# Kernel optimization log

Measured on AMD Instinct MI355X. Metric: run time of the kernel, lower is better.

Reference implementation:

```python
import jax, jax.numpy as jnp
import numpy as np

B, C, H, W = 4, 512, 32, 32
NUM_HEADS, DIM_HEAD = 16, 32
DIM_ATTN = NUM_HEADS * DIM_HEAD  # 512
N = H * W


def setup_inputs() -> dict:
    key = jax.random.key(0)
    ks = jax.random.split(key, 6)
    s = 0.02
    return {
        "x": jax.random.normal(ks[0], (B, C, H, W), jnp.float32),
        "w_qkv": jax.random.normal(ks[1], (3 * DIM_ATTN, C), jnp.float32) * s,
        "b_qkv": jax.random.normal(ks[2], (3 * DIM_ATTN,), jnp.float32) * s,
        "w_proj": jax.random.normal(ks[3], (C, DIM_ATTN), jnp.float32) * s,
        "b_proj": jax.random.normal(ks[4], (C,), jnp.float32) * s,
        "shared_rel_pos": jax.random.normal(ks[5], (1, NUM_HEADS, N, N), jnp.float32) * s,
    }


def reference(x, w_qkv, b_qkv, w_proj, b_proj, shared_rel_pos):
    b, c, h, w = x.shape
    n = h * w
    scale = DIM_HEAD ** -0.5
    # 1x1 conv == per-pixel matmul over channels
    qkv = jnp.einsum('bchw,oc->bohw', x, w_qkv) + b_qkv[None, :, None, None]
    # [B, heads, 3*dh, N] -> chunk along dim 2 (matches torch .chunk(3, dim=2))
    qkv = qkv.reshape(b, NUM_HEADS, 3 * DIM_HEAD, n)
    q, k, v = jnp.split(qkv, 3, axis=2)          # each [B, heads, dh, N]
    attn = jnp.einsum('bhdi,bhdj->bhij', q, k) * scale  # q^T @ k
    attn = attn + shared_rel_pos
    attn = jax.nn.softmax(attn, axis=-1)
    out = jnp.einsum('bhdj,bhij->bhdi', v, attn)  # v @ attn^T, [B, heads, dh, N]
    out = out.reshape(b, NUM_HEADS * DIM_HEAD, h, w)
    out = jnp.einsum('bchw,oc->bohw', out, w_proj) + b_proj[None, :, None, None]
    return out
```

## Files before the change

### kernel.cpp

```cpp
#include <hip/hip_runtime.h>
#include <cstdint>
#include <cstddef>

#define BATCH 4
#define CIN   512
#define NPIX  1024
#define HEADS 16
#define DH    32
#define DATTN 512
#define O_QKV 1536

typedef unsigned short u16;
typedef __bf16 bf16x4 __attribute__((ext_vector_type(4)));
typedef __bf16 bf16x8 __attribute__((ext_vector_type(8)));
typedef float  f32x4  __attribute__((ext_vector_type(4)));

typedef const __attribute__((address_space(1))) void g1_t;
typedef __attribute__((address_space(3))) void l3_t;

#if defined(__has_builtin)
#if __has_builtin(__builtin_amdgcn_exp2f)
#define EXP2(x) __builtin_amdgcn_exp2f(x)
#endif
#endif
#ifndef EXP2
#define EXP2(x) __expf((x) * 0.6931471805599453f)
#endif

__device__ __forceinline__ u16 f2bf(float f) {
  unsigned u = __float_as_uint(f);
  u += 0x7fffu + ((u >> 16) & 1u);
  return (u16)(u >> 16);
}

__device__ __forceinline__ void gl_lds16(const void* gp, void* lp) {
  __builtin_amdgcn_global_load_lds((g1_t*)gp, (l3_t*)lp, 16, 0, 0);
}

__global__ __launch_bounds__(256) void prep_w(const float* __restrict__ w1,
                                              const float* __restrict__ w2,
                                              u16* __restrict__ o1,
                                              u16* __restrict__ o2) {
  const int idx = blockIdx.x * 256 + threadIdx.x;
  const int n1 = (O_QKV * CIN) >> 2;
  float4 v = (idx < n1) ? reinterpret_cast<const float4*>(w1)[idx]
                        : reinterpret_cast<const float4*>(w2)[idx - n1];
  uint2 pk = make_uint2((unsigned)f2bf(v.x) | ((unsigned)f2bf(v.y) << 16),
                        (unsigned)f2bf(v.z) | ((unsigned)f2bf(v.w) << 16));
  if (idx < n1) reinterpret_cast<uint2*>(o1)[idx] = pk;
  else          reinterpret_cast<uint2*>(o2)[idx - n1] = pk;
}

__global__ __launch_bounds__(256) void prep_x(const float* __restrict__ x,
                                              u16* __restrict__ xt) {
  __shared__ float sT[64][65];
  const int t  = threadIdx.x;
  const int n0 = blockIdx.x * 64;
  const int c0 = blockIdx.y * 64;
  const int b  = blockIdx.z;
  const float* xb = x + ((size_t)b * CIN + c0) * NPIX + n0;
#pragma unroll
  for (int i = 0; i < 4; ++i) {
    int r   = i * 16 + (t >> 4);
    int col = (t & 15) << 2;
    float4 v = *reinterpret_cast<const float4*>(&xb[(size_t)r * NPIX + col]);
    sT[r][col + 0] = v.x; sT[r][col + 1] = v.y;
    sT[r][col + 2] = v.z; sT[r][col + 3] = v.w;
  }
  __syncthreads();
#pragma unroll
  for (int i = 0; i < 2; ++i) {
    int nl = t >> 2;
    int ch = (t & 3) + (i << 2);
    u16 tmp[8];
#pragma unroll
    for (int e = 0; e < 8; ++e) tmp[e] = f2bf(sT[(ch << 3) + e][nl]);
    *reinterpret_cast<uint4*>(&xt[((size_t)b * NPIX + n0 + nl) * CIN + c0 + (ch << 3)]) =
        *reinterpret_cast<uint4*>(tmp);
  }
}

__global__ __launch_bounds__(256) void gemm_qkv_mfma(const u16* __restrict__ wq,
                                                     const u16* __restrict__ xt,
                                                     const float* __restrict__ bias,
                                                     u16* __restrict__ qt,
                                                     u16* __restrict__ kt,
                                                     u16* __restrict__ vt) {
  __shared__ __align__(16) u16 sA[96 * 64];
  __shared__ __align__(16) u16 sB[128 * 64];
  const int t  = threadIdx.x;
  const int w  = t >> 6, l = t & 63, g = l >> 4, ln = l & 15;
  const int n0 = blockIdx.x * 128;
  const int h  = blockIdx.y;
  const int b  = blockIdx.z;
  const int wm = w >> 1, wn = w & 1;

  const u16* wbase = wq + (size_t)h * 96 * CIN;
  const u16* xbase = xt + ((size_t)b * NPIX + n0) * CIN;

  f32x4 acc[3][4];
#pragma unroll
  for (int mi = 0; mi < 3; ++mi)
#pragma unroll
    for (int ni = 0; ni < 4; ++ni) acc[mi][ni] = {0.f, 0.f, 0.f, 0.f};

  for (int k0 = 0; k0 < CIN; k0 += 64) {
#pragma unroll
    for (int i = 0; i < 3; ++i) {
      int chunk = i * 256 + (w << 6) + l;
      gl_lds16(wbase + ((size_t)(chunk >> 3)) * CIN + k0 + ((chunk & 7) << 3),
               (char*)sA + i * 4096 + (w << 10));
    }
#pragma unroll
    for (int i = 0; i < 4; ++i) {
      int chunk = i * 256 + (w << 6) + l;
      gl_lds16(xbase + ((size_t)(chunk >> 3)) * CIN + k0 + ((chunk & 7) << 3),
               (char*)sB + i * 4096 + (w << 10));
    }
    __syncthreads();
#pragma unroll
    for (int kk = 0; kk < 64; kk += 32) {
      bf16x8 af[3], bfr[4];
#pragma unroll
      for (int mi = 0; mi < 3; ++mi)
        af[mi] = *reinterpret_cast<const bf16x8*>(&sA[(48 * wm + 16 * mi + ln) * 64 + kk + (g << 3)]);
#pragma unroll
      for (int ni = 0; ni < 4; ++ni)
        bfr[ni] = *reinterpret_cast<const bf16x8*>(&sB[((wn << 6) + (ni << 4) + ln) * 64 + kk + (g << 3)]);
#pragma unroll
      for (int mi = 0; mi < 3; ++mi)
#pragma unroll
        for (int ni = 0; ni < 4; ++ni)
          acc[mi][ni] = __builtin_amdgcn_mfma_f32_16x16x32_bf16(af[mi], bfr[ni], acc[mi][ni], 0, 0, 0);
    }
    __syncthreads();
  }

  const float QSC = 0.17677669529663687f * 1.4426950408889634f;
  const float* bh = bias + h * 96;
#pragma unroll
  for (int mi = 0; mi < 3; ++mi) {
    const int sec = 48 * wm + 16 * mi;
    const int rb  = sec + (g << 2);
    const float b0 = bh[rb + 0], b1 = bh[rb + 1], b2 = bh[rb + 2], b3 = bh[rb + 3];
#pragma unroll
    for (int ni = 0; ni < 4; ++ni) {
      const int n = n0 + (wn << 6) + (ni << 4) + ln;
      f32x4 a = acc[mi][ni];
      float v0 = a[0] + b0, v1 = a[1] + b1, v2 = a[2] + b2, v3 = a[3] + b3;
      if (sec < 32) { v0 *= QSC; v1 *= QSC; v2 *= QSC; v3 *= QSC; }
      u16 e0 = f2bf(v0), e1 = f2bf(v1), e2 = f2bf(v2), e3 = f2bf(v3);
      if (sec < 32) {
        const int d = sec + (g << 2);
        uint2 pk = make_uint2((unsigned)e0 | ((unsigned)e1 << 16),
                              (unsigned)e2 | ((unsigned)e3 << 16));
        *reinterpret_cast<uint2*>(&qt[(((size_t)(b * HEADS + h)) * NPIX + n) * DH + d]) = pk;
      } else if (sec < 64) {
        const int d = sec - 32 + (g << 2);
        uint2 pk = make_uint2((unsigned)e0 | ((unsigned)e1 << 16),
                              (unsigned)e2 | ((unsigned)e3 << 16));
        *reinterpret_cast<uint2*>(&kt[(((size_t)(b * HEADS + h)) * NPIX + n) * DH + d]) = pk;
      } else {
        const int d = sec - 64 + (g << 2);
        u16* vp = &vt[(((size_t)(b * HEADS + h)) * DH + d) * NPIX + n];
        vp[0] = e0; vp[NPIX] = e1; vp[2 * NPIX] = e2; vp[3 * NPIX] = e3;
      }
    }
  }
}

__global__ __launch_bounds__(256, 4) void attn_mfma(const u16* __restrict__ qt,
                                                    const u16* __restrict__ kt,
                                                    const u16* __restrict__ vt,
                                                    const float* __restrict__ rel,
                                                    u16* __restrict__ aout) {
  __shared__ __align__(16) u16 sK[2][2048];
  __shared__ __align__(16) u16 sV[2][2048];
  __shared__ __align__(16) u16 sP[4][1024];

  const int t  = threadIdx.x;
  const int w  = t >> 6, l = t & 63, g = l >> 4, ln = l & 15;
  const int bid = blockIdx.x;
  const int xcd = bid & 7, sl = bid >> 3;
  const int b   = sl & 3;
  const int i0  = ((sl >> 2) & 15) << 6;
  const int h   = (xcd << 1) | (sl >> 6);
  const int iw  = w;

  const size_t bh = (size_t)(b * HEADS + h);

  const int sc_r  = t >> 3;
  const int sc_kc = (t & 7) ^ (sc_r & 7) ^ ((sc_r >> 3) & 1);
  const int sc_vc = (t & 7) ^ (sc_r & 7);
  const u16* ksrc = kt + (bh * NPIX + ((sc_r << 1) | (sc_kc >> 2))) * DH +
                    ((sc_kc & 3) << 3);
  const u16* vsrc = vt + (bh * DH + sc_r) * NPIX + (sc_vc << 3);
  char* kdst = (char*)&sK[0][0] + (w << 10);
  char* vdst = (char*)&sV[0][0] + (w << 10);

#define STAGE(s_, p_) do {                                          \
    gl_lds16(ksrc + (size_t)(s_) * 2048, kdst + (p_) * 4096);       \
    gl_lds16(vsrc + (size_t)(s_) * 64,   vdst + (p_) * 4096);       \
  } while (0)

  STAGE(0, 0);

  bf16x8 qf = *reinterpret_cast<const bf16x8*>(
      qt + (bh * NPIX + i0 + (iw << 4) + ln) * DH + (g << 3));

  const float* relp = rel + ((size_t)h * NPIX + i0 + (iw << 4) + (g << 2)) * NPIX +
                      (ln << 2);
  f32x4 relA4[4], relB4[4];
#pragma unroll
  for (int v = 0; v < 4; ++v)
    relA4[v] = *reinterpret_cast<const f32x4*>(relp + (size_t)v * NPIX);

  f32x4 vzero = {0.f, 0.f, 0.f, 0.f};
  f32x4 accO[2] = {vzero, vzero};
  f32x4 l_lane = vzero;

  u16* sPw = &sP[w][0];
  const float LOG2E = 1.4426950408889634f;

  for (int s = 0; s < 16; ++s) {
    const int p = s & 1;
    __syncthreads();
    if (s < 15) {
      STAGE(s + 1, p ^ 1);
#pragma unroll
      for (int v = 0; v < 4; ++v)
        relB4[v] = *reinterpret_cast<const f32x4*>(relp + (size_t)v * NPIX + ((s + 1) << 6));
    }

    const u16* Kb = &sK[p][0];
    const u16* Vb = &sV[p][0];

    f32x4 sfr[4];
    __builtin_amdgcn_s_setprio(1);
#pragma unroll
    for (int jj = 0; jj < 4; ++jj) {
      const int r  = (ln << 1) + (jj >> 1);
      const int ks = ((((jj & 1) << 2) | g) ^ (r & 7)) ^ ((r >> 3) & 1);
      bf16x8 kf = *reinterpret_cast<const bf16x8*>(Kb + r * 64 + ks * 8);
      sfr[jj] = __builtin_amdgcn_mfma_f32_16x16x32_bf16(qf, kf, vzero, 0, 0, 0);
    }
    __builtin_amdgcn_s_setprio(0);

#pragma unroll
    for (int v = 0; v < 4; ++v) {
      float p0 = EXP2(fmaf(relA4[v][0], LOG2E, sfr[0][v]));
      float p1 = EXP2(fmaf(relA4[v][1], LOG2E, sfr[1][v]));
      float p2 = EXP2(fmaf(relA4[v][2], LOG2E, sfr[2][v]));
      float p3 = EXP2(fmaf(relA4[v][3], LOG2E, sfr[3][v]));
      l_lane[v] += (p0 + p1) + (p2 + p3);
      bf16x4 pk;
      pk[0] = (__bf16)p0; pk[1] = (__bf16)p1; pk[2] = (__bf16)p2; pk[3] = (__bf16)p3;
      const int rw = (g << 2) + v;
      *reinterpret_cast<bf16x4*>(
          sPw + rw * 64 + ((((ln >> 1) ^ (rw & 7)) << 3) | ((ln & 1) << 2))) = pk;
    }

    __builtin_amdgcn_s_setprio(1);
#pragma unroll
    for (int kc = 0; kc < 2; ++kc) {
      const int lc = (kc << 2) | g;
      bf16x8 pa = *reinterpret_cast<const bf16x8*>(sPw + ln * 64 + ((lc ^ (ln & 7)) << 3));
#pragma unroll
      for (int dc = 0; dc < 2; ++dc) {
        const int d  = (dc << 4) + ln;
        const int vs = lc ^ (d & 7);
        bf16x8 vf = *reinterpret_cast<const bf16x8*>(Vb + d * 64 + vs * 8);
        accO[dc] = __builtin_amdgcn_mfma_f32_16x16x32_bf16(pa, vf, accO[dc], 0, 0, 0);
      }
    }
    __builtin_amdgcn_s_setprio(0);

    if (s < 15) {
#pragma unroll
      for (int v = 0; v < 4; ++v) relA4[v] = relB4[v];
    }
  }
#undef STAGE

#pragma unroll
  for (int v = 0; v < 4; ++v) {
    float ls = l_lane[v];
    ls += __shfl_xor(ls, 1);
    ls += __shfl_xor(ls, 2);
    ls += __shfl_xor(ls, 4);
    ls += __shfl_xor(ls, 8);
    const float inv = 1.f / ls;
    const size_t row = (size_t)b * NPIX + i0 + (iw << 4) + (g << 2) + v;
    aout[row * DATTN + (h << 5) + ln]      = f2bf(accO[0][v] * inv);
    aout[row * DATTN + (h << 5) + 16 + ln] = f2bf(accO[1][v] * inv);
  }
}

__global__ __launch_bounds__(256) void gemm_proj_mfma(const u16* __restrict__ wp,
                                                      const u16* __restrict__ at,
                                                      const float* __restrict__ bias,
                                                      float* __restrict__ out) {
  __shared__ __align__(16) u16 sA[64 * 64];
  __shared__ __align__(16) u16 sB[128 * 64];
  const int t  = threadIdx.x;
  const int w  = t >> 6, l = t & 63, g = l >> 4, ln = l & 15;
  const int n0 = blockIdx.x * 128;
  const int o0 = blockIdx.y * 64;
  const int b  = blockIdx.z;
  const int wm = w >> 1, wn = w & 1;

  const u16* wbase = wp + (size_t)o0 * DATTN;
  const u16* abase = at + ((size_t)b * NPIX + n0) * DATTN;

  f32x4 acc[2][4];
#pragma unroll
  for (int mi = 0; mi < 2; ++mi)
#pragma unroll
    for (int ni = 0; ni < 4; ++ni) acc[mi][ni] = {0.f, 0.f, 0.f, 0.f};

  for (int k0 = 0; k0 < DATTN; k0 += 64) {
#pragma unroll
    for (int i = 0; i < 2; ++i) {
      int chunk = i * 256 + (w << 6) + l;
      gl_lds16(wbase + ((size_t)(chunk >> 3)) * DATTN + k0 + ((chunk & 7) << 3),
               (char*)sA + i * 4096 + (w << 10));
    }
#pragma unroll
    for (int i = 0; i < 4; ++i) {
      int chunk = i * 256 + (w << 6) + l;
      gl_lds16(abase + ((size_t)(chunk >> 3)) * DATTN + k0 + ((chunk & 7) << 3),
               (char*)sB + i * 4096 + (w << 10));
    }
    __syncthreads();
#pragma unroll
    for (int kk = 0; kk < 64; kk += 32) {
      bf16x8 af[2], bfr[4];
#pragma unroll
      for (int mi = 0; mi < 2; ++mi)
        af[mi] = *reinterpret_cast<const bf16x8*>(&sA[((wm << 5) + (mi << 4) + ln) * 64 + kk + (g << 3)]);
#pragma unroll
      for (int ni = 0; ni < 4; ++ni)
        bfr[ni] = *reinterpret_cast<const bf16x8*>(&sB[((wn << 6) + (ni << 4) + ln) * 64 + kk + (g << 3)]);
#pragma unroll
      for (int mi = 0; mi < 2; ++mi)
#pragma unroll
        for (int ni = 0; ni < 4; ++ni)
          acc[mi][ni] = __builtin_amdgcn_mfma_f32_16x16x32_bf16(af[mi], bfr[ni], acc[mi][ni], 0, 0, 0);
    }
    __syncthreads();
  }

#pragma unroll
  for (int mi = 0; mi < 2; ++mi) {
    const int o = o0 + (wm << 5) + (mi << 4) + (g << 2);
    const float b0 = bias[o], b1 = bias[o + 1], b2 = bias[o + 2], b3 = bias[o + 3];
#pragma unroll
    for (int ni = 0; ni < 4; ++ni) {
      const int n = n0 + (wn << 6) + (ni << 4) + ln;
      float* op = &out[((size_t)b * DATTN + o) * NPIX + n];
      op[0]        = acc[mi][ni][0] + b0;
      op[NPIX]     = acc[mi][ni][1] + b1;
      op[2 * NPIX] = acc[mi][ni][2] + b2;
      op[3 * NPIX] = acc[mi][ni][3] + b3;
    }
  }
}

extern "C" void kernel_launch(void* const* d_in, const int* in_sizes, int n_in,
                              void* d_out, int out_size, void* d_ws, size_t ws_size,
                              hipStream_t stream) {
  (void)in_sizes; (void)n_in; (void)out_size; (void)ws_size;
  const float* x      = (const float*)d_in[0];
  const float* w_qkv  = (const float*)d_in[1];
  const float* b_qkv  = (const float*)d_in[2];
  const float* w_proj = (const float*)d_in[3];
  const float* b_proj = (const float*)d_in[4];
  const float* rel    = (const float*)d_in[5];
  float* out = (float*)d_out;

  u16* xt    = (u16*)d_ws;
  u16* wq_bf = xt + (size_t)BATCH * NPIX * CIN;
  u16* wp_bf = wq_bf + (size_t)O_QKV * CIN;
  u16* qt    = wp_bf + (size_t)DATTN * DATTN;
  u16* kt    = qt + (size_t)BATCH * HEADS * NPIX * DH;
  u16* vt    = kt + (size_t)BATCH * HEADS * NPIX * DH;
  u16* aout  = vt + (size_t)BATCH * HEADS * NPIX * DH;

  prep_w<<<1024, 256, 0, stream>>>(w_qkv, w_proj, wq_bf, wp_bf);
  prep_x<<<dim3(NPIX / 64, CIN / 64, BATCH), 256, 0, stream>>>(x, xt);
  gemm_qkv_mfma<<<dim3(NPIX / 128, HEADS, BATCH), 256, 0, stream>>>(wq_bf, xt, b_qkv, qt, kt, vt);
  attn_mfma<<<1024, 256, 0, stream>>>(qt, kt, vt, rel, aout);
  gemm_proj_mfma<<<dim3(NPIX / 128, DATTN / 64, BATCH), 256, 0, stream>>>(wp_bf, aout, b_proj, out);
}
```

Measured before the change: 63.92 us.

## Load K and V fragments directly from global into registers, dropping LDS staging

The attention kernel no longer stages K and V tiles through double-buffered shared memory with async global-to-LDS copies and a per-step __syncthreads. Each wave now reads its MFMA K fragments (prefetched one step ahead into registers) and V fragments straight from global memory. This removes LDS traffic and block-wide barriers, but each of the four waves now fetches the same K/V data separately, and V loads are issued in the same iteration they are used, so there is less reuse and more latency exposure on L2/global reads. Register pressure also rises with the extra prefetch fragments.

Result: slower. 104.4 us (+63.2%).

```diff
diff --git a/kernel.cpp b/kernel.cpp
--- a/kernel.cpp
+++ b/kernel.cpp
@@ -174,8 +174,6 @@
                                                     const u16* __restrict__ vt,
                                                     const float* __restrict__ rel,
                                                     u16* __restrict__ aout) {
-  __shared__ __align__(16) u16 sK[2][2048];
-  __shared__ __align__(16) u16 sV[2][2048];
   __shared__ __align__(16) u16 sP[4][1024];
 
   const int t  = threadIdx.x;
@@ -189,31 +187,14 @@
 
   const size_t bh = (size_t)(b * HEADS + h);
 
-  const int sc_r  = t >> 3;
-  const int sc_kc = (t & 7) ^ (sc_r & 7) ^ ((sc_r >> 3) & 1);
-  const int sc_vc = (t & 7) ^ (sc_r & 7);
-  const u16* ksrc = kt + (bh * NPIX + ((sc_r << 1) | (sc_kc >> 2))) * DH +
-                    ((sc_kc & 3) << 3);
-  const u16* vsrc = vt + (bh * DH + sc_r) * NPIX + (sc_vc << 3);
-  char* kdst = (char*)&sK[0][0] + (w << 10);
-  char* vdst = (char*)&sV[0][0] + (w << 10);
-
-#define STAGE(s_, p_) do {                                          \
-    gl_lds16(ksrc + (size_t)(s_) * 2048, kdst + (p_) * 4096);       \
-    gl_lds16(vsrc + (size_t)(s_) * 64,   vdst + (p_) * 4096);       \
-  } while (0)
-
-  STAGE(0, 0);
-
   bf16x8 qf = *reinterpret_cast<const bf16x8*>(
       qt + (bh * NPIX + i0 + (iw << 4) + ln) * DH + (g << 3));
 
+  const u16* kbase = kt + (bh * NPIX + (ln << 2)) * DH + (g << 3);
+  const u16* vbase0 = vt + (bh * DH + ln) * NPIX + (g << 3);
+  const u16* vbase1 = vbase0 + 16 * NPIX;
   const float* relp = rel + ((size_t)h * NPIX + i0 + (iw << 4) + (g << 2)) * NPIX +
                       (ln << 2);
-  f32x4 relA4[4], relB4[4];
-#pragma unroll
-  for (int v = 0; v < 4; ++v)
-    relA4[v] = *reinterpret_cast<const f32x4*>(relp + (size_t)v * NPIX);
 
   f32x4 vzero = {0.f, 0.f, 0.f, 0.f};
   f32x4 accO[2] = {vzero, vzero};
@@ -222,36 +203,51 @@
   u16* sPw = &sP[w][0];
   const float LOG2E = 1.4426950408889634f;
 
+  const int paOff0 = ln * 64 + ((g ^ (ln & 7)) << 3);
+  const int paOff1 = ln * 64 + (((4 | g) ^ (ln & 7)) << 3);
+
+  bf16x8 kA0, kA1, kA2, kA3, kB0, kB1, kB2, kB3;
+  f32x4 relA4[4], relB4[4];
+  kA0 = *reinterpret_cast<const bf16x8*>(kbase);
+  kA1 = *reinterpret_cast<const bf16x8*>(kbase + DH);
+  kA2 = *reinterpret_cast<const bf16x8*>(kbase + 2 * DH);
+  kA3 = *reinterpret_cast<const bf16x8*>(kbase + 3 * DH);
+#pragma unroll
+  for (int v = 0; v < 4; ++v)
+    relA4[v] = *reinterpret_cast<const f32x4*>(relp + (size_t)v * NPIX);
+
   for (int s = 0; s < 16; ++s) {
-    const int p = s & 1;
-    __syncthreads();
     if (s < 15) {
-      STAGE(s + 1, p ^ 1);
+      const u16* kn = kbase + (size_t)(s + 1) * 64 * DH;
+      kB0 = *reinterpret_cast<const bf16x8*>(kn);
+      kB1 = *reinterpret_cast<const bf16x8*>(kn + DH);
+      kB2 = *reinterpret_cast<const bf16x8*>(kn + 2 * DH);
+      kB3 = *reinterpret_cast<const bf16x8*>(kn + 3 * DH);
 #pragma unroll
       for (int v = 0; v < 4; ++v)
         relB4[v] = *reinterpret_cast<const f32x4*>(relp + (size_t)v * NPIX + ((s + 1) << 6));
     }
-
-    const u16* Kb = &sK[p][0];
-    const u16* Vb = &sV[p][0];
-
-    f32x4 sfr[4];
+    const u16* vp0 = vbase0 + (s << 6);
+    const u16* vp1 = vbase1 + (s << 6);
+    bf16x8 vf00 = *reinterpret_cast<const bf16x8*>(vp0);
+    bf16x8 vf01 = *reinterpret_cast<const bf16x8*>(vp1);
+    bf16x8 vf10 = *reinterpret_cast<const bf16x8*>(vp0 + 32);
+    bf16x8 vf11 = *reinterpret_cast<const bf16x8*>(vp1 + 32);
+
+    f32x4 sfr0, sfr1, sfr2, sfr3;
     __builtin_amdgcn_s_setprio(1);
-#pragma unroll
-    for (int jj = 0; jj < 4; ++jj) {
-      const int r  = (ln << 1) + (jj >> 1);
-      const int ks = ((((jj & 1) << 2) | g) ^ (r & 7)) ^ ((r >> 3) & 1);
-      bf16x8 kf = *reinterpret_cast<const bf16x8*>(Kb + r * 64 + ks * 8);
-      sfr[jj] = __builtin_amdgcn_mfma_f32_16x16x32_bf16(qf, kf, vzero, 0, 0, 0);
-    }
+    sfr0 = __builtin_amdgcn_mfma_f32_16x16x32_bf16(qf, kA0, vzero, 0, 0, 0);
+    sfr1 = __builtin_amdgcn_mfma_f32_16x16x32_bf16(qf, kA1, vzero, 0, 0, 0);
+    sfr2 = __builtin_amdgcn_mfma_f32_16x16x32_bf16(qf, kA2, vzero, 0, 0, 0);
+    sfr3 = __builtin_amdgcn_mfma_f32_16x16x32_bf16(qf, kA3, vzero, 0, 0, 0);
     __builtin_amdgcn_s_setprio(0);
 
 #pragma unroll
     for (int v = 0; v < 4; ++v) {
-      float p0 = EXP2(fmaf(relA4[v][0], LOG2E, sfr[0][v]));
-      float p1 = EXP2(fmaf(relA4[v][1], LOG2E, sfr[1][v]));
-      float p2 = EXP2(fmaf(relA4[v][2], LOG2E, sfr[2][v]));
-      float p3 = EXP2(fmaf(relA4[v][3], LOG2E, sfr[3][v]));
+      float p0 = EXP2(fmaf(relA4[v][0], LOG2E, sfr0[v]));
+      float p1 = EXP2(fmaf(relA4[v][1], LOG2E, sfr1[v]));
+      float p2 = EXP2(fmaf(relA4[v][2], LOG2E, sfr2[v]));
+      float p3 = EXP2(fmaf(relA4[v][3], LOG2E, sfr3[v]));
       l_lane[v] += (p0 + p1) + (p2 + p3);
       bf16x4 pk;
       pk[0] = (__bf16)p0; pk[1] = (__bf16)p1; pk[2] = (__bf16)p2; pk[3] = (__bf16)p3;
@@ -261,26 +257,22 @@
     }
 
     __builtin_amdgcn_s_setprio(1);
-#pragma unroll
-    for (int kc = 0; kc < 2; ++kc) {
-      const int lc = (kc << 2) | g;
-      bf16x8 pa = *reinterpret_cast<const bf16x8*>(sPw + ln * 64 + ((lc ^ (ln & 7)) << 3));
-#pragma unroll
-      for (int dc = 0; dc < 2; ++dc) {
-        const int d  = (dc << 4) + ln;
-        const int vs = lc ^ (d & 7);
-        bf16x8 vf = *reinterpret_cast<const bf16x8*>(Vb + d * 64 + vs * 8);
-        accO[dc] = __builtin_amdgcn_mfma_f32_16x16x32_bf16(pa, vf, accO[dc], 0, 0, 0);
-      }
+    {
+      bf16x8 pa0 = *reinterpret_cast<const bf16x8*>(sPw + paOff0);
+      accO[0] = __builtin_amdgcn_mfma_f32_16x16x32_bf16(pa0, vf00, accO[0], 0, 0, 0);
+      accO[1] = __builtin_amdgcn_mfma_f32_16x16x32_bf16(pa0, vf01, accO[1], 0, 0, 0);
+      bf16x8 pa1 = *reinterpret_cast<const bf16x8*>(sPw + paOff1);
+      accO[0] = __builtin_amdgcn_mfma_f32_16x16x32_bf16(pa1, vf10, accO[0], 0, 0, 0);
+      accO[1] = __builtin_amdgcn_mfma_f32_16x16x32_bf16(pa1, vf11, accO[1], 0, 0, 0);
     }
     __builtin_amdgcn_s_setprio(0);
 
     if (s < 15) {
+      kA0 = kB0; kA1 = kB1; kA2 = kB2; kA3 = kB3;
 #pragma unroll
       for (int v = 0; v < 4; ++v) relA4[v] = relB4[v];
     }
   }
-#undef STAGE
 
 #pragma unroll
   for (int v = 0; v < 4; ++v) {
```

## Fuse prep kernels and double attention key tile per pipeline stage

Applied to the files above, without the earlier changes.

Merges the weight-cast and x-transpose prep kernels into one launch, removing a kernel launch and its gap. In the attention kernel, each pipeline stage now covers 128 keys instead of 64, halving the number of barrier-synchronized iterations and issuing more MFMAs per sync. The rel-pos bias is now loaded synchronously inside each iteration instead of being prefetched one stage ahead, which may expose global latency. LDS use doubles, which can reduce occupancy.

After: 63.93 us. About the same (+0.0%).

```diff
diff --git a/kernel.cpp b/kernel.cpp
--- a/kernel.cpp
+++ b/kernel.cpp
@@ -37,46 +37,48 @@
   __builtin_amdgcn_global_load_lds((g1_t*)gp, (l3_t*)lp, 16, 0, 0);
 }
 
-__global__ __launch_bounds__(256) void prep_w(const float* __restrict__ w1,
-                                              const float* __restrict__ w2,
-                                              u16* __restrict__ o1,
-                                              u16* __restrict__ o2) {
-  const int idx = blockIdx.x * 256 + threadIdx.x;
-  const int n1 = (O_QKV * CIN) >> 2;
-  float4 v = (idx < n1) ? reinterpret_cast<const float4*>(w1)[idx]
-                        : reinterpret_cast<const float4*>(w2)[idx - n1];
-  uint2 pk = make_uint2((unsigned)f2bf(v.x) | ((unsigned)f2bf(v.y) << 16),
-                        (unsigned)f2bf(v.z) | ((unsigned)f2bf(v.w) << 16));
-  if (idx < n1) reinterpret_cast<uint2*>(o1)[idx] = pk;
-  else          reinterpret_cast<uint2*>(o2)[idx - n1] = pk;
-}
-
-__global__ __launch_bounds__(256) void prep_x(const float* __restrict__ x,
-                                              u16* __restrict__ xt) {
-  __shared__ float sT[64][65];
-  const int t  = threadIdx.x;
-  const int n0 = blockIdx.x * 64;
-  const int c0 = blockIdx.y * 64;
-  const int b  = blockIdx.z;
-  const float* xb = x + ((size_t)b * CIN + c0) * NPIX + n0;
-#pragma unroll
-  for (int i = 0; i < 4; ++i) {
-    int r   = i * 16 + (t >> 4);
-    int col = (t & 15) << 2;
-    float4 v = *reinterpret_cast<const float4*>(&xb[(size_t)r * NPIX + col]);
-    sT[r][col + 0] = v.x; sT[r][col + 1] = v.y;
-    sT[r][col + 2] = v.z; sT[r][col + 3] = v.w;
-  }
-  __syncthreads();
-#pragma unroll
-  for (int i = 0; i < 2; ++i) {
-    int nl = t >> 2;
-    int ch = (t & 3) + (i << 2);
-    u16 tmp[8];
-#pragma unroll
-    for (int e = 0; e < 8; ++e) tmp[e] = f2bf(sT[(ch << 3) + e][nl]);
-    *reinterpret_cast<uint4*>(&xt[((size_t)b * NPIX + n0 + nl) * CIN + c0 + (ch << 3)]) =
-        *reinterpret_cast<uint4*>(tmp);
+__global__ __launch_bounds__(256) void prep_fused(const float* __restrict__ x,
+                                                  const float* __restrict__ w1,
+                                                  const float* __restrict__ w2,
+                                                  u16* __restrict__ xt,
+                                                  u16* __restrict__ o1,
+                                                  u16* __restrict__ o2) {
+  const int t = threadIdx.x;
+  if (blockIdx.x < 512) {
+    __shared__ float sT[64][65];
+    const int q  = blockIdx.x;
+    const int n0 = (q & 15) << 6;
+    const int c0 = ((q >> 4) & 7) << 6;
+    const int b  = q >> 7;
+    const float* xb = x + ((size_t)b * CIN + c0) * NPIX + n0;
+#pragma unroll
+    for (int i = 0; i < 4; ++i) {
+      int r   = i * 16 + (t >> 4);
+      int col = (t & 15) << 2;
+      float4 v = *reinterpret_cast<const float4*>(&xb[(size_t)r * NPIX + col]);
+      sT[r][col + 0] = v.x; sT[r][col + 1] = v.y;
+      sT[r][col + 2] = v.z; sT[r][col + 3] = v.w;
+    }
+    __syncthreads();
+#pragma unroll
+    for (int i = 0; i < 2; ++i) {
+      int nl = t >> 2;
+      int ch = (t & 3) + (i << 2);
+      u16 tmp[8];
+#pragma unroll
+      for (int e = 0; e < 8; ++e) tmp[e] = f2bf(sT[(ch << 3) + e][nl]);
+      *reinterpret_cast<uint4*>(&xt[((size_t)b * NPIX + n0 + nl) * CIN + c0 + (ch << 3)]) =
+          *reinterpret_cast<uint4*>(tmp);
+    }
+  } else {
+    const int idx = (blockIdx.x - 512) * 256 + t;
+    const int n1 = (O_QKV * CIN) >> 2;
+    float4 v = (idx < n1) ? reinterpret_cast<const float4*>(w1)[idx]
+                          : reinterpret_cast<const float4*>(w2)[idx - n1];
+    uint2 pk = make_uint2((unsigned)f2bf(v.x) | ((unsigned)f2bf(v.y) << 16),
+                          (unsigned)f2bf(v.z) | ((unsigned)f2bf(v.w) << 16));
+    if (idx < n1) reinterpret_cast<uint2*>(o1)[idx] = pk;
+    else          reinterpret_cast<uint2*>(o2)[idx - n1] = pk;
   }
 }
 
@@ -174,9 +176,9 @@
                                                     const u16* __restrict__ vt,
                                                     const float* __restrict__ rel,
                                                     u16* __restrict__ aout) {
-  __shared__ __align__(16) u16 sK[2][2048];
-  __shared__ __align__(16) u16 sV[2][2048];
-  __shared__ __align__(16) u16 sP[4][1024];
+  __shared__ __align__(16) u16 sK[2][4096];
+  __shared__ __align__(16) u16 sV[2][4096];
+  __shared__ __align__(16) u16 sP[4][2048];
 
   const int t  = threadIdx.x;
   const int w  = t >> 6, l = t & 63, g = l >> 4, ln = l & 15;
@@ -198,9 +200,11 @@
   char* kdst = (char*)&sK[0][0] + (w << 10);
   char* vdst = (char*)&sV[0][0] + (w << 10);
 
-#define STAGE(s_, p_) do {                                          \
-    gl_lds16(ksrc + (size_t)(s_) * 2048, kdst + (p_) * 4096);       \
-    gl_lds16(vsrc + (size_t)(s_) * 64,   vdst + (p_) * 4096);       \
+#define STAGE(s_, p_) do {                                                  \
+    gl_lds16(ksrc + (size_t)(s_) * 4096,        kdst + (p_) * 8192);        \
+    gl_lds16(ksrc + (size_t)(s_) * 4096 + 2048, kdst + (p_) * 8192 + 4096); \
+    gl_lds16(vsrc + (size_t)(s_) * 128,         vdst + (p_) * 8192);        \
+    gl_lds16(vsrc + (size_t)(s_) * 128 + 64,    vdst + (p_) * 8192 + 4096); \
   } while (0)
 
   STAGE(0, 0);
@@ -210,10 +214,6 @@
 
   const float* relp = rel + ((size_t)h * NPIX + i0 + (iw << 4) + (g << 2)) * NPIX +
                       (ln << 2);
-  f32x4 relA4[4], relB4[4];
-#pragma unroll
-  for (int v = 0; v < 4; ++v)
-    relA4[v] = *reinterpret_cast<const f32x4*>(relp + (size_t)v * NPIX);
 
   f32x4 vzero = {0.f, 0.f, 0.f, 0.f};
   f32x4 accO[2] = {vzero, vzero};
@@ -222,63 +222,72 @@
   u16* sPw = &sP[w][0];
   const float LOG2E = 1.4426950408889634f;
 
-  for (int s = 0; s < 16; ++s) {
+  for (int s = 0; s < 8; ++s) {
     const int p = s & 1;
     __syncthreads();
-    if (s < 15) {
-      STAGE(s + 1, p ^ 1);
+    if (s < 7) STAGE(s + 1, p ^ 1);
+
+    f32x4 relv[2][4];
+#pragma unroll
+    for (int hh = 0; hh < 2; ++hh)
 #pragma unroll
       for (int v = 0; v < 4; ++v)
-        relB4[v] = *reinterpret_cast<const f32x4*>(relp + (size_t)v * NPIX + ((s + 1) << 6));
-    }
+        relv[hh][v] = *reinterpret_cast<const f32x4*>(
+            relp + (size_t)v * NPIX + (s << 7) + (hh << 6));
 
     const u16* Kb = &sK[p][0];
     const u16* Vb = &sV[p][0];
 
-    f32x4 sfr[4];
+    f32x4 sfr[8];
     __builtin_amdgcn_s_setprio(1);
 #pragma unroll
-    for (int jj = 0; jj < 4; ++jj) {
-      const int r  = (ln << 1) + (jj >> 1);
-      const int ks = ((((jj & 1) << 2) | g) ^ (r & 7)) ^ ((r >> 3) & 1);
-      bf16x8 kf = *reinterpret_cast<const bf16x8*>(Kb + r * 64 + ks * 8);
+    for (int jj = 0; jj < 8; ++jj) {
+      const int hh = jj >> 2, q = jj & 3;
+      const int r  = (ln << 1) + (q >> 1);
+      const int ks = ((((q & 1) << 2) | g) ^ (r & 7)) ^ ((r >> 3) & 1);
+      bf16x8 kf = *reinterpret_cast<const bf16x8*>(Kb + (hh << 11) + r * 64 + ks * 8);
       sfr[jj] = __builtin_amdgcn_mfma_f32_16x16x32_bf16(qf, kf, vzero, 0, 0, 0);
     }
     __builtin_amdgcn_s_setprio(0);
 
 #pragma unroll
     for (int v = 0; v < 4; ++v) {
-      float p0 = EXP2(fmaf(relA4[v][0], LOG2E, sfr[0][v]));
-      float p1 = EXP2(fmaf(relA4[v][1], LOG2E, sfr[1][v]));
-      float p2 = EXP2(fmaf(relA4[v][2], LOG2E, sfr[2][v]));
-      float p3 = EXP2(fmaf(relA4[v][3], LOG2E, sfr[3][v]));
+      const int rw = (g << 2) + v;
+      const int pwoff = rw * 64 + ((((ln >> 1) ^ (rw & 7)) << 3) | ((ln & 1) << 2));
+      float p0 = EXP2(fmaf(relv[0][v][0], LOG2E, sfr[0][v]));
+      float p1 = EXP2(fmaf(relv[0][v][1], LOG2E, sfr[1][v]));
+      float p2 = EXP2(fmaf(relv[0][v][2], LOG2E, sfr[2][v]));
+      float p3 = EXP2(fmaf(relv[0][v][3], LOG2E, sfr[3][v]));
       l_lane[v] += (p0 + p1) + (p2 + p3);
       bf16x4 pk;
       pk[0] = (__bf16)p0; pk[1] = (__bf16)p1; pk[2] = (__bf16)p2; pk[3] = (__bf16)p3;
-      const int rw = (g << 2) + v;
-      *reinterpret_cast<bf16x4*>(
-          sPw + rw * 64 + ((((ln >> 1) ^ (rw & 7)) << 3) | ((ln & 1) << 2))) = pk;
+      *reinterpret_cast<bf16x4*>(sPw + pwoff) = pk;
+      float p4 = EXP2(fmaf(relv[1][v][0], LOG2E, sfr[4][v]));
+      float p5 = EXP2(fmaf(relv[1][v][1], LOG2E, sfr[5][v]));
+      float p6 = EXP2(fmaf(relv[1][v][2], LOG2E, sfr[6][v]));
+      float p7 = EXP2(fmaf(relv[1][v][3], LOG2E, sfr[7][v]));
+      l_lane[v] += (p4 + p5) + (p6 + p7);
+      bf16x4 pk2;
+      pk2[0] = (__bf16)p4; pk2[1] = (__bf16)p5; pk2[2] = (__bf16)p6; pk2[3] = (__bf16)p7;
+      *reinterpret_cast<bf16x4*>(sPw + 1024 + pwoff) = pk2;
     }
 
     __builtin_amdgcn_s_setprio(1);
 #pragma unroll
-    for (int kc = 0; kc < 2; ++kc) {
-      const int lc = (kc << 2) | g;
-      bf16x8 pa = *reinterpret_cast<const bf16x8*>(sPw + ln * 64 + ((lc ^ (ln & 7)) << 3));
+    for (int c = 0; c < 4; ++c) {
+      const int hh = c >> 1, kc2 = c & 1;
+      const int lc = (kc2 << 2) | g;
+      bf16x8 pa = *reinterpret_cast<const bf16x8*>(
+          sPw + (hh << 10) + ln * 64 + ((lc ^ (ln & 7)) << 3));
 #pragma unroll
       for (int dc = 0; dc < 2; ++dc) {
         const int d  = (dc << 4) + ln;
         const int vs = lc ^ (d & 7);
-        bf16x8 vf = *reinterpret_cast<const bf16x8*>(Vb + d * 64 + vs * 8);
+        bf16x8 vf = *reinterpret_cast<const bf16x8*>(Vb + (hh << 11) + d * 64 + vs * 8);
         accO[dc] = __builtin_amdgcn_mfma_f32_16x16x32_bf16(pa, vf, accO[dc], 0, 0, 0);
       }
     }
     __builtin_amdgcn_s_setprio(0);
-
-    if (s < 15) {
-#pragma unroll
-      for (int v = 0; v < 4; ++v) relA4[v] = relB4[v];
-    }
   }
 #undef STAGE
 
@@ -386,8 +395,7 @@
   u16* vt    = kt + (size_t)BATCH * HEADS * NPIX * DH;
   u16* aout  = vt + (size_t)BATCH * HEADS * NPIX * DH;
 
-  prep_w<<<1024, 256, 0, stream>>>(w_qkv, w_proj, wq_bf, wp_bf);
-  prep_x<<<dim3(NPIX / 64, CIN / 64, BATCH), 256, 0, stream>>>(x, xt);
+  prep_fused<<<1536, 256, 0, stream>>>(x, w_qkv, w_proj, xt, wq_bf, wp_bf);
   gemm_qkv_mfma<<<dim3(NPIX / 128, HEADS, BATCH), 256, 0, stream>>>(wq_bf, xt, b_qkv, qt, kt, vt);
   attn_mfma<<<1024, 256, 0, stream>>>(qt, kt, vt, rel, aout);
   gemm_proj_mfma<<<dim3(NPIX / 128, DATTN / 64, BATCH), 256, 0, stream>>>(wp_bf, aout, b_proj, out);
```

## Share rel_pos loads across two batches per attention block and fuse prep kernels

Applied to the files above, without the earlier changes.

Each attention block now handles two batch elements for the same head and query tile. The shared_rel_pos fp32 tile is therefore read once and reused for both, which halves traffic on the largest input. The grid shrinks to 512 blocks, LDS for K/V doubles, and launch bounds drop to 2 waves, so occupancy and parallelism go down. The weight and x bf16 preparation kernels are also merged into one launch to save a kernel launch.

New measurement: 62.74 us. Within noise of the previous version (-1.8%).

```diff
diff --git a/kernel.cpp b/kernel.cpp
--- a/kernel.cpp
+++ b/kernel.cpp
@@ -37,46 +37,48 @@
   __builtin_amdgcn_global_load_lds((g1_t*)gp, (l3_t*)lp, 16, 0, 0);
 }
 
-__global__ __launch_bounds__(256) void prep_w(const float* __restrict__ w1,
-                                              const float* __restrict__ w2,
-                                              u16* __restrict__ o1,
-                                              u16* __restrict__ o2) {
-  const int idx = blockIdx.x * 256 + threadIdx.x;
-  const int n1 = (O_QKV * CIN) >> 2;
-  float4 v = (idx < n1) ? reinterpret_cast<const float4*>(w1)[idx]
-                        : reinterpret_cast<const float4*>(w2)[idx - n1];
-  uint2 pk = make_uint2((unsigned)f2bf(v.x) | ((unsigned)f2bf(v.y) << 16),
-                        (unsigned)f2bf(v.z) | ((unsigned)f2bf(v.w) << 16));
-  if (idx < n1) reinterpret_cast<uint2*>(o1)[idx] = pk;
-  else          reinterpret_cast<uint2*>(o2)[idx - n1] = pk;
-}
-
-__global__ __launch_bounds__(256) void prep_x(const float* __restrict__ x,
-                                              u16* __restrict__ xt) {
-  __shared__ float sT[64][65];
-  const int t  = threadIdx.x;
-  const int n0 = blockIdx.x * 64;
-  const int c0 = blockIdx.y * 64;
-  const int b  = blockIdx.z;
-  const float* xb = x + ((size_t)b * CIN + c0) * NPIX + n0;
-#pragma unroll
-  for (int i = 0; i < 4; ++i) {
-    int r   = i * 16 + (t >> 4);
-    int col = (t & 15) << 2;
-    float4 v = *reinterpret_cast<const float4*>(&xb[(size_t)r * NPIX + col]);
-    sT[r][col + 0] = v.x; sT[r][col + 1] = v.y;
-    sT[r][col + 2] = v.z; sT[r][col + 3] = v.w;
-  }
-  __syncthreads();
-#pragma unroll
-  for (int i = 0; i < 2; ++i) {
-    int nl = t >> 2;
-    int ch = (t & 3) + (i << 2);
-    u16 tmp[8];
-#pragma unroll
-    for (int e = 0; e < 8; ++e) tmp[e] = f2bf(sT[(ch << 3) + e][nl]);
-    *reinterpret_cast<uint4*>(&xt[((size_t)b * NPIX + n0 + nl) * CIN + c0 + (ch << 3)]) =
-        *reinterpret_cast<uint4*>(tmp);
+__global__ __launch_bounds__(256) void prep_fused(const float* __restrict__ x,
+                                                  const float* __restrict__ w1,
+                                                  const float* __restrict__ w2,
+                                                  u16* __restrict__ xt,
+                                                  u16* __restrict__ o1,
+                                                  u16* __restrict__ o2) {
+  const int t = threadIdx.x;
+  if (blockIdx.x < 512) {
+    __shared__ float sT[64][65];
+    const int q  = blockIdx.x;
+    const int n0 = (q & 15) << 6;
+    const int c0 = ((q >> 4) & 7) << 6;
+    const int b  = q >> 7;
+    const float* xb = x + ((size_t)b * CIN + c0) * NPIX + n0;
+#pragma unroll
+    for (int i = 0; i < 4; ++i) {
+      int r   = i * 16 + (t >> 4);
+      int col = (t & 15) << 2;
+      float4 v = *reinterpret_cast<const float4*>(&xb[(size_t)r * NPIX + col]);
+      sT[r][col + 0] = v.x; sT[r][col + 1] = v.y;
+      sT[r][col + 2] = v.z; sT[r][col + 3] = v.w;
+    }
+    __syncthreads();
+#pragma unroll
+    for (int i = 0; i < 2; ++i) {
+      int nl = t >> 2;
+      int ch = (t & 3) + (i << 2);
+      u16 tmp[8];
+#pragma unroll
+      for (int e = 0; e < 8; ++e) tmp[e] = f2bf(sT[(ch << 3) + e][nl]);
+      *reinterpret_cast<uint4*>(&xt[((size_t)b * NPIX + n0 + nl) * CIN + c0 + (ch << 3)]) =
+          *reinterpret_cast<uint4*>(tmp);
+    }
+  } else {
+    const int idx = (blockIdx.x - 512) * 256 + t;
+    const int n1 = (O_QKV * CIN) >> 2;
+    float4 v = (idx < n1) ? reinterpret_cast<const float4*>(w1)[idx]
+                          : reinterpret_cast<const float4*>(w2)[idx - n1];
+    uint2 pk = make_uint2((unsigned)f2bf(v.x) | ((unsigned)f2bf(v.y) << 16),
+                          (unsigned)f2bf(v.z) | ((unsigned)f2bf(v.w) << 16));
+    if (idx < n1) reinterpret_cast<uint2*>(o1)[idx] = pk;
+    else          reinterpret_cast<uint2*>(o2)[idx - n1] = pk;
   }
 }
 
@@ -169,44 +171,51 @@
   }
 }
 
-__global__ __launch_bounds__(256, 4) void attn_mfma(const u16* __restrict__ qt,
+__global__ __launch_bounds__(256, 2) void attn_mfma(const u16* __restrict__ qt,
                                                     const u16* __restrict__ kt,
                                                     const u16* __restrict__ vt,
                                                     const float* __restrict__ rel,
                                                     u16* __restrict__ aout) {
-  __shared__ __align__(16) u16 sK[2][2048];
-  __shared__ __align__(16) u16 sV[2][2048];
+  __shared__ __align__(16) u16 sK[2][2][2048];
+  __shared__ __align__(16) u16 sV[2][2][2048];
   __shared__ __align__(16) u16 sP[4][1024];
 
   const int t  = threadIdx.x;
   const int w  = t >> 6, l = t & 63, g = l >> 4, ln = l & 15;
   const int bid = blockIdx.x;
   const int xcd = bid & 7, sl = bid >> 3;
-  const int b   = sl & 3;
-  const int i0  = ((sl >> 2) & 15) << 6;
-  const int h   = (xcd << 1) | (sl >> 6);
+  const int bp  = sl & 1;
+  const int i0  = ((sl >> 1) & 15) << 6;
+  const int h   = (xcd << 1) | (sl >> 5);
   const int iw  = w;
 
-  const size_t bh = (size_t)(b * HEADS + h);
+  const size_t bh0 = (size_t)((bp * 2 + 0) * HEADS + h);
+  const size_t bh1 = (size_t)((bp * 2 + 1) * HEADS + h);
 
   const int sc_r  = t >> 3;
   const int sc_kc = (t & 7) ^ (sc_r & 7) ^ ((sc_r >> 3) & 1);
   const int sc_vc = (t & 7) ^ (sc_r & 7);
-  const u16* ksrc = kt + (bh * NPIX + ((sc_r << 1) | (sc_kc >> 2))) * DH +
-                    ((sc_kc & 3) << 3);
-  const u16* vsrc = vt + (bh * DH + sc_r) * NPIX + (sc_vc << 3);
-  char* kdst = (char*)&sK[0][0] + (w << 10);
-  char* vdst = (char*)&sV[0][0] + (w << 10);
-
-#define STAGE(s_, p_) do {                                          \
-    gl_lds16(ksrc + (size_t)(s_) * 2048, kdst + (p_) * 4096);       \
-    gl_lds16(vsrc + (size_t)(s_) * 64,   vdst + (p_) * 4096);       \
+  const size_t kro = ((size_t)((sc_r << 1) | (sc_kc >> 2))) * DH + ((sc_kc & 3) << 3);
+  const u16* ksrc0 = kt + bh0 * NPIX * DH + kro;
+  const u16* ksrc1 = kt + bh1 * NPIX * DH + kro;
+  const u16* vsrc0 = vt + (bh0 * DH + sc_r) * NPIX + (sc_vc << 3);
+  const u16* vsrc1 = vt + (bh1 * DH + sc_r) * NPIX + (sc_vc << 3);
+  char* kBase = (char*)&sK[0][0][0] + (w << 10);
+  char* vBase = (char*)&sV[0][0][0] + (w << 10);
+
+#define STAGE(s_, p_) do {                                               \
+    gl_lds16(ksrc0 + (size_t)(s_) * 2048, kBase + (p_) * 8192);          \
+    gl_lds16(ksrc1 + (size_t)(s_) * 2048, kBase + (p_) * 8192 + 4096);   \
+    gl_lds16(vsrc0 + (size_t)(s_) * 64,   vBase + (p_) * 8192);          \
+    gl_lds16(vsrc1 + (size_t)(s_) * 64,   vBase + (p_) * 8192 + 4096);   \
   } while (0)
 
   STAGE(0, 0);
 
-  bf16x8 qf = *reinterpret_cast<const bf16x8*>(
-      qt + (bh * NPIX + i0 + (iw << 4) + ln) * DH + (g << 3));
+  bf16x8 qf0 = *reinterpret_cast<const bf16x8*>(
+      qt + (bh0 * NPIX + i0 + (iw << 4) + ln) * DH + (g << 3));
+  bf16x8 qf1 = *reinterpret_cast<const bf16x8*>(
+      qt + (bh1 * NPIX + i0 + (iw << 4) + ln) * DH + (g << 3));
 
   const float* relp = rel + ((size_t)h * NPIX + i0 + (iw << 4) + (g << 2)) * NPIX +
                       (ln << 2);
@@ -216,8 +225,9 @@
     relA4[v] = *reinterpret_cast<const f32x4*>(relp + (size_t)v * NPIX);
 
   f32x4 vzero = {0.f, 0.f, 0.f, 0.f};
-  f32x4 accO[2] = {vzero, vzero};
-  f32x4 l_lane = vzero;
+  f32x4 accO0[2] = {vzero, vzero};
+  f32x4 accO1[2] = {vzero, vzero};
+  f32x4 l_lane0 = vzero, l_lane1 = vzero;
 
   u16* sPw = &sP[w][0];
   const float LOG2E = 1.4426950408889634f;
@@ -232,48 +242,54 @@
         relB4[v] = *reinterpret_cast<const f32x4*>(relp + (size_t)v * NPIX + ((s + 1) << 6));
     }
 
-    const u16* Kb = &sK[p][0];
-    const u16* Vb = &sV[p][0];
-
-    f32x4 sfr[4];
-    __builtin_amdgcn_s_setprio(1);
-#pragma unroll
-    for (int jj = 0; jj < 4; ++jj) {
-      const int r  = (ln << 1) + (jj >> 1);
-      const int ks = ((((jj & 1) << 2) | g) ^ (r & 7)) ^ ((r >> 3) & 1);
-      bf16x8 kf = *reinterpret_cast<const bf16x8*>(Kb + r * 64 + ks * 8);
-      sfr[jj] = __builtin_amdgcn_mfma_f32_16x16x32_bf16(qf, kf, vzero, 0, 0, 0);
-    }
-    __builtin_amdgcn_s_setprio(0);
-
-#pragma unroll
-    for (int v = 0; v < 4; ++v) {
-      float p0 = EXP2(fmaf(relA4[v][0], LOG2E, sfr[0][v]));
-      float p1 = EXP2(fmaf(relA4[v][1], LOG2E, sfr[1][v]));
-      float p2 = EXP2(fmaf(relA4[v][2], LOG2E, sfr[2][v]));
-      float p3 = EXP2(fmaf(relA4[v][3], LOG2E, sfr[3][v]));
-      l_lane[v] += (p0 + p1) + (p2 + p3);
-      bf16x4 pk;
-      pk[0] = (__bf16)p0; pk[1] = (__bf16)p1; pk[2] = (__bf16)p2; pk[3] = (__bf16)p3;
-      const int rw = (g << 2) + v;
-      *reinterpret_cast<bf16x4*>(
-          sPw + rw * 64 + ((((ln >> 1) ^ (rw & 7)) << 3) | ((ln & 1) << 2))) = pk;
-    }
-
-    __builtin_amdgcn_s_setprio(1);
-#pragma unroll
-    for (int kc = 0; kc < 2; ++kc) {
-      const int lc = (kc << 2) | g;
-      bf16x8 pa = *reinterpret_cast<const bf16x8*>(sPw + ln * 64 + ((lc ^ (ln & 7)) << 3));
-#pragma unroll
-      for (int dc = 0; dc < 2; ++dc) {
-        const int d  = (dc << 4) + ln;
-        const int vs = lc ^ (d & 7);
-        bf16x8 vf = *reinterpret_cast<const bf16x8*>(Vb + d * 64 + vs * 8);
-        accO[dc] = __builtin_amdgcn_mfma_f32_16x16x32_bf16(pa, vf, accO[dc], 0, 0, 0);
+#pragma unroll
+    for (int b2 = 0; b2 < 2; ++b2) {
+      const u16* Kb = &sK[p][b2][0];
+      const u16* Vb = &sV[p][b2][0];
+      const bf16x8 qf = b2 ? qf1 : qf0;
+
+      f32x4 sfr[4];
+      __builtin_amdgcn_s_setprio(1);
+#pragma unroll
+      for (int jj = 0; jj < 4; ++jj) {
+        const int r  = (ln << 1) + (jj >> 1);
+        const int ks = ((((jj & 1) << 2) | g) ^ (r & 7)) ^ ((r >> 3) & 1);
+        bf16x8 kf = *reinterpret_cast<const bf16x8*>(Kb + r * 64 + ks * 8);
+        sfr[jj] = __builtin_amdgcn_mfma_f32_16x16x32_bf16(qf, kf, vzero, 0, 0, 0);
       }
-    }
-    __builtin_amdgcn_s_setprio(0);
+      __builtin_amdgcn_s_setprio(0);
+
+#pragma unroll
+      for (int v = 0; v < 4; ++v) {
+        float p0 = EXP2(fmaf(relA4[v][0], LOG2E, sfr[0][v]));
+        float p1 = EXP2(fmaf(relA4[v][1], LOG2E, sfr[1][v]));
+        float p2 = EXP2(fmaf(relA4[v][2], LOG2E, sfr[2][v]));
+        float p3 = EXP2(fmaf(relA4[v][3], LOG2E, sfr[3][v]));
+        if (b2) l_lane1[v] += (p0 + p1) + (p2 + p3);
+        else    l_lane0[v] += (p0 + p1) + (p2 + p3);
+        bf16x4 pk;
+        pk[0] = (__bf16)p0; pk[1] = (__bf16)p1; pk[2] = (__bf16)p2; pk[3] = (__bf16)p3;
+        const int rw = (g << 2) + v;
+        *reinterpret_cast<bf16x4*>(
+            sPw + rw * 64 + ((((ln >> 1) ^ (rw & 7)) << 3) | ((ln & 1) << 2))) = pk;
+      }
+
+      __builtin_amdgcn_s_setprio(1);
+#pragma unroll
+      for (int kc = 0; kc < 2; ++kc) {
+        const int lc = (kc << 2) | g;
+        bf16x8 pa = *reinterpret_cast<const bf16x8*>(sPw + ln * 64 + ((lc ^ (ln & 7)) << 3));
+#pragma unroll
+        for (int dc = 0; dc < 2; ++dc) {
+          const int d  = (dc << 4) + ln;
+          const int vs = lc ^ (d & 7);
+          bf16x8 vf = *reinterpret_cast<const bf16x8*>(Vb + d * 64 + vs * 8);
+          if (b2) accO1[dc] = __builtin_amdgcn_mfma_f32_16x16x32_bf16(pa, vf, accO1[dc], 0, 0, 0);
+          else    accO0[dc] = __builtin_amdgcn_mfma_f32_16x16x32_bf16(pa, vf, accO0[dc], 0, 0, 0);
+        }
+      }
+      __builtin_amdgcn_s_setprio(0);
+    }
 
     if (s < 15) {
 #pragma unroll
@@ -284,15 +300,27 @@
 
 #pragma unroll
   for (int v = 0; v < 4; ++v) {
-    float ls = l_lane[v];
+    float ls = l_lane0[v];
     ls += __shfl_xor(ls, 1);
     ls += __shfl_xor(ls, 2);
     ls += __shfl_xor(ls, 4);
     ls += __shfl_xor(ls, 8);
     const float inv = 1.f / ls;
-    const size_t row = (size_t)b * NPIX + i0 + (iw << 4) + (g << 2) + v;
-    aout[row * DATTN + (h << 5) + ln]      = f2bf(accO[0][v] * inv);
-    aout[row * DATTN + (h << 5) + 16 + ln] = f2bf(accO[1][v] * inv);
+    const size_t row = (size_t)(bp * 2 + 0) * NPIX + i0 + (iw << 4) + (g << 2) + v;
+    aout[row * DATTN + (h << 5) + ln]      = f2bf(accO0[0][v] * inv);
+    aout[row * DATTN + (h << 5) + 16 + ln] = f2bf(accO0[1][v] * inv);
+  }
+#pragma unroll
+  for (int v = 0; v < 4; ++v) {
+    float ls = l_lane1[v];
+    ls += __shfl_xor(ls, 1);
+    ls += __shfl_xor(ls, 2);
+    ls += __shfl_xor(ls, 4);
+    ls += __shfl_xor(ls, 8);
+    const float inv = 1.f / ls;
+    const size_t row = (size_t)(bp * 2 + 1) * NPIX + i0 + (iw << 4) + (g << 2) + v;
+    aout[row * DATTN + (h << 5) + ln]      = f2bf(accO1[0][v] * inv);
+    aout[row * DATTN + (h << 5) + 16 + ln] = f2bf(accO1[1][v] * inv);
   }
 }
 
@@ -386,9 +414,8 @@
   u16* vt    = kt + (size_t)BATCH * HEADS * NPIX * DH;
   u16* aout  = vt + (size_t)BATCH * HEADS * NPIX * DH;
 
-  prep_w<<<1024, 256, 0, stream>>>(w_qkv, w_proj, wq_bf, wp_bf);
-  prep_x<<<dim3(NPIX / 64, CIN / 64, BATCH), 256, 0, stream>>>(x, xt);
+  prep_fused<<<1536, 256, 0, stream>>>(x, w_qkv, w_proj, xt, wq_bf, wp_bf);
   gemm_qkv_mfma<<<dim3(NPIX / 128, HEADS, BATCH), 256, 0, stream>>>(wq_bf, xt, b_qkv, qt, kt, vt);
-  attn_mfma<<<1024, 256, 0, stream>>>(qt, kt, vt, rel, aout);
+  attn_mfma<<<512, 256, 0, stream>>>(qt, kt, vt, rel, aout);
   gemm_proj_mfma<<<dim3(NPIX / 128, DATTN / 64, BATCH), 256, 0, stream>>>(wp_bf, aout, b_proj, out);
 }
```
